# Performance work log

Measured on AMD Instinct MI355X. Metric: run time of the kernel, lower is better.

## Reference

```python
import jax, jax.numpy as jnp
import numpy as np

B, S, D, H = 1, 4096, 768, 12
HD = D // H  # 64

def setup_inputs() -> dict:
    key = jax.random.key(0)
    k1, k2, k3 = jax.random.split(key, 3)
    x = jax.random.normal(k1, (B, S, D), dtype=jnp.float32)
    W_attn = jax.random.normal(k2, (D, 3 * D), dtype=jnp.float32) * 0.02
    b_attn = jnp.zeros((3 * D,), dtype=jnp.float32)
    W_proj = jax.random.normal(k3, (D, D), dtype=jnp.float32) * 0.02
    b_proj = jnp.zeros((D,), dtype=jnp.float32)
    return {"x": x, "W_attn": W_attn, "b_attn": b_attn, "W_proj": W_proj, "b_proj": b_proj}

def reference(x, W_attn, b_attn, W_proj, b_proj):
    # qkv projection (Conv1D = x @ W + b)
    qkv = x @ W_attn + b_attn  # [B,S,3D]
    q, k, v = jnp.split(qkv, 3, axis=-1)
    def split_heads(t):
        return t.reshape(B, S, H, HD).transpose(0, 2, 1, 3)  # [B,H,S,HD]
    q, k, v = split_heads(q), split_heads(k), split_heads(v)
    # NOTE: original applies no 1/sqrt(head_dim) scaling
    scores = jnp.einsum('bhqd,bhkd->bhqk', q, k)  # [B,H,S,S]
    causal = jnp.tril(jnp.ones((S, S), dtype=bool))
    mask_value = jnp.finfo(scores.dtype).min
    scores = jnp.where(causal, scores, mask_value)
    attn = jax.nn.softmax(scores, axis=-1)
    # dropout is identity in eval mode
    out = jnp.einsum('bhqk,bhkd->bhqd', attn, v)  # [B,H,S,HD]
    out = out.transpose(0, 2, 1, 3).reshape(B, S, D)
    return out @ W_proj + b_proj
```

## Files before the change

kernel.cpp:

```cpp
#include <hip/hip_runtime.h>


typedef short bf16x8 __attribute__((ext_vector_type(8)));
typedef float f32x4 __attribute__((ext_vector_type(4)));
typedef unsigned short u16x8_t __attribute__((ext_vector_type(8)));
typedef unsigned short u16x4_t __attribute__((ext_vector_type(4)));

#define ATT_S  4096
#define ATT_D  768
#define ATT_3D 2304
#define ATT_H  12
#define LOG2E  1.44269504089f

__device__ __forceinline__ unsigned short f2b(float f) {
  union { float f; unsigned int u; } v; v.f = f;
  unsigned int r = v.u + 0x7fffu + ((v.u >> 16) & 1u);
  return (unsigned short)(r >> 16);
}
__device__ __forceinline__ float b2f(unsigned short b) {
  union { unsigned int u; float f; } v; v.u = ((unsigned int)b) << 16;
  return v.f;
}

__device__ __forceinline__ f32x4 mfma16(bf16x8 a, bf16x8 b, f32x4 c) {
  return __builtin_amdgcn_mfma_f32_16x16x32_bf16(a, b, c, 0, 0, 0);
}

__device__ __forceinline__ void glds16(const void* g, void* l) {
  __builtin_amdgcn_global_load_lds((__attribute__((address_space(1))) void*)g,
                                   (__attribute__((address_space(3))) void*)l,
                                   16, 0, 0);
}

__device__ __forceinline__ int swz8(int row, int c) {
  return row * 64 + ((c ^ (row & 7)) << 3);
}


__global__ __launch_bounds__(256) void convert_f32_bf16(
    const float* __restrict__ in, unsigned short* __restrict__ out, int n4) {
  int i = blockIdx.x * 256 + threadIdx.x;
  if (i >= n4) return;
  float4 v = ((const float4*)in)[i];
  u16x4_t o;
  o[0] = f2b(v.x); o[1] = f2b(v.y); o[2] = f2b(v.z); o[3] = f2b(v.w);
  ((u16x4_t*)out)[i] = o;
}

__global__ __launch_bounds__(256) void transpose_conv(
    const float* __restrict__ W, unsigned short* __restrict__ WT, int K, int N) {
  __shared__ float tile[32][33];
  int bx = blockIdx.x, by = blockIdx.y;
  int tx = threadIdx.x & 31, ty = threadIdx.x >> 5;
#pragma unroll
  for (int k = 0; k < 4; k++)
    tile[ty + k * 8][tx] = W[(size_t)(by * 32 + ty + k * 8) * N + bx * 32 + tx];
  __syncthreads();
#pragma unroll
  for (int k = 0; k < 4; k++)
    WT[(size_t)(bx * 32 + ty + k * 8) * K + by * 32 + tx] = f2b(tile[tx][ty + k * 8]);
}


template <int BF16_OUT>
__global__ __launch_bounds__(256) void gemm_bias(
    const unsigned short* __restrict__ A, const unsigned short* __restrict__ Bt,
    const float* __restrict__ bias, void* __restrict__ Cout,
    int M, int N, int K) {
  __shared__ unsigned short As[128 * 32];
  __shared__ unsigned short Bs[128 * 32];
  const int t = threadIdx.x;
  const int lane = t & 63;
  const int wave = t >> 6;
  const int wr = wave >> 1, wc = wave & 1;
  const int rl = lane & 15, rg = lane >> 4;

  const int nbn = N >> 7;
  const int nwg = gridDim.x;
  const int bid = blockIdx.x;
  const int cpx = nwg >> 3;
  const int swz = (bid & 7) * cpx + (bid >> 3);
  const int bm = swz / nbn, bn = swz % nbn;

  const unsigned short* Ab = A + (size_t)bm * 128 * K;
  const unsigned short* Bb = Bt + (size_t)bn * 128 * K;

  f32x4 acc[4][4];
#pragma unroll
  for (int m = 0; m < 4; m++)
#pragma unroll
    for (int n = 0; n < 4; n++) acc[m][n] = (f32x4){0.f, 0.f, 0.f, 0.f};

  for (int kt = 0; kt < K; kt += 32) {
    if (kt) __syncthreads();
#pragma unroll
    for (int it = 0; it < 2; ++it) {
      int idx = it * 256 + t;
      int row = idx >> 2;
      int slot = idx & 3;
      int sl2 = slot ^ ((row >> 1) & 3);
      unsigned short* ldsA = As + (size_t)(it * 256 + wave * 64) * 8;
      unsigned short* ldsB = Bs + (size_t)(it * 256 + wave * 64) * 8;
      glds16(Ab + (size_t)row * K + kt + sl2 * 8, ldsA);
      glds16(Bb + (size_t)row * K + kt + sl2 * 8, ldsB);
    }
    __syncthreads();

    bf16x8 a[4], b[4];
#pragma unroll
    for (int m = 0; m < 4; m++) {
      int row = wr * 64 + m * 16 + rl;
      int sl2 = rg ^ ((row >> 1) & 3);
      a[m] = *(const bf16x8*)&As[row * 32 + sl2 * 8];
    }
#pragma unroll
    for (int n = 0; n < 4; n++) {
      int row = wc * 64 + n * 16 + rl;
      int sl2 = rg ^ ((row >> 1) & 3);
      b[n] = *(const bf16x8*)&Bs[row * 32 + sl2 * 8];
    }
#pragma unroll
    for (int m = 0; m < 4; m++)
#pragma unroll
      for (int n = 0; n < 4; n++)
        acc[m][n] = mfma16(a[m], b[n], acc[m][n]);
  }

#pragma unroll
  for (int n = 0; n < 4; n++) {
    int col = bn * 128 + wc * 64 + n * 16 + rl;
    float bv = bias[col];
#pragma unroll
    for (int m = 0; m < 4; m++) {
      int row0 = bm * 128 + wr * 64 + m * 16 + rg * 4;
#pragma unroll
      for (int i = 0; i < 4; i++) {
        float v = acc[m][n][i] + bv;
        if (BF16_OUT)
          ((unsigned short*)Cout)[(size_t)(row0 + i) * N + col] = f2b(v);
        else
          ((float*)Cout)[(size_t)(row0 + i) * N + col] = v;
      }
    }
  }
}


__global__ __launch_bounds__(256) void attn_fwd(
    const unsigned short* __restrict__ qkv, unsigned short* __restrict__ aout,
    unsigned short* __restrict__ pscr, float* __restrict__ ml) {
  __shared__ unsigned short Kb[64 * 64];
  __shared__ unsigned short Vb[64 * 64];
  __shared__ unsigned short Ps[4][16 * 64];

  const int tid = threadIdx.x;
  const int lane = tid & 63;
  const int w = tid >> 6;
  const int rl = lane & 15, rg = lane >> 4;

  const int bid = blockIdx.x;
  const int h = bid % ATT_H;
  const int u = 159 - (bid / ATT_H);
  int qb, ck;
  if (u < 16)      { qb = u;                 ck = 0; }
  else if (u < 48) { qb = 16 + ((u - 16) >> 1); ck = (u - 16) & 1; }
  else if (u < 96) { qb = 32 + (u - 48) / 3;    ck = (u - 48) % 3; }
  else             { qb = 48 + ((u - 96) >> 2); ck = (u - 96) & 3; }

  const int nt = qb + 1;
  const int t0 = ck * 16;
  const int t1 = min(nt, t0 + 16);
  const int qbase = qb * 64 + w * 16;

  unsigned short* Pw = Ps[w];
  const int skey = lane >> 3;
  const int slot = lane & 7;

  bf16x8 qf[2];
#pragma unroll
  for (int ks = 0; ks < 2; ks++)
    qf[ks] = *(const bf16x8*)&qkv[(size_t)(qbase + rl) * ATT_3D + h * 64 + ks * 32 + rg * 8];

  float mS = -3.0e38f, lS = 0.f;
  f32x4 oacc[4];
#pragma unroll
  for (int hf = 0; hf < 4; hf++) oacc[hf] = (f32x4){0.f, 0.f, 0.f, 0.f};

  u16x8_t kr[2], vr[2];
  const size_t gstep = (size_t)64 * ATT_3D;
  size_t gbase = (size_t)(w * 8 + skey) * ATT_3D + 768 + h * 64 + slot * 8;

#pragma unroll
  for (int it = 0; it < 2; ++it) {
    kr[it] = *(const u16x8_t*)&qkv[gbase + (size_t)t0 * gstep + it * 32 * ATT_3D];
    vr[it] = *(const u16x8_t*)&qkv[gbase + (size_t)t0 * gstep + it * 32 * ATT_3D + 768];
  }
  {
#pragma unroll
    for (int it = 0; it < 2; ++it) {
      int key = it * 32 + w * 8 + skey;
      *(u16x8_t*)&Kb[swz8(key, slot)] = kr[it];
      *(u16x8_t*)&Pw[swz8(it * 8 + skey, slot)] = vr[it];
    }
#pragma unroll
    for (int kk = 0; kk < 2; ++kk) {
      u16x8_t g;
#pragma unroll
      for (int j = 0; j < 8; j++)
        g[j] = Pw[swz8(kk * 8 + j, lane >> 3) + (lane & 7)];
      *(u16x8_t*)&Vb[swz8(lane, kk * 4 + w)] = g;
    }
  }
  __syncthreads();

  for (int t = t0; t < t1; ++t) {
    const bool pref = (t + 1 < t1);
    if (pref) {
      size_t gb = gbase + (size_t)(t + 1) * gstep;
#pragma unroll
      for (int it = 0; it < 2; ++it) {
        kr[it] = *(const u16x8_t*)&qkv[gb + it * 32 * ATT_3D];
        vr[it] = *(const u16x8_t*)&qkv[gb + it * 32 * ATT_3D + 768];
      }
    }

    f32x4 st[4];
#pragma unroll
    for (int kf = 0; kf < 4; kf++) st[kf] = (f32x4){0.f, 0.f, 0.f, 0.f};
    __builtin_amdgcn_s_setprio(1);
#pragma unroll
    for (int ks = 0; ks < 2; ks++) {
#pragma unroll
      for (int kf = 0; kf < 4; kf++) {
        bf16x8 kfr = *(const bf16x8*)&Kb[swz8(kf * 16 + rl, ks * 4 + rg)];
        st[kf] = mfma16(kfr, qf[ks], st[kf]);
      }
    }
    __builtin_amdgcn_s_setprio(0);

    __syncthreads();
    if (pref) {
#pragma unroll
      for (int it = 0; it < 2; ++it)
        *(u16x8_t*)&Kb[swz8(it * 32 + w * 8 + skey, slot)] = kr[it];
    }

    if (t == nt - 1) {
#pragma unroll
      for (int kf = 0; kf < 4; kf++)
#pragma unroll
        for (int i = 0; i < 4; i++) {
          int key = t * 64 + kf * 16 + rg * 4 + i;
          if (key > qbase + rl) st[kf][i] = -3.0e38f;
        }
    }

    float pm = fmaxf(fmaxf(st[0][0], st[0][1]), fmaxf(st[0][2], st[0][3]));
#pragma unroll
    for (int kf = 1; kf < 4; kf++)
      pm = fmaxf(pm, fmaxf(fmaxf(st[kf][0], st[kf][1]),
                           fmaxf(st[kf][2], st[kf][3])));
    pm = fmaxf(pm, __shfl_xor(pm, 16, 64));
    pm = fmaxf(pm, __shfl_xor(pm, 32, 64));
    if (!__all(pm - mS <= 8.f)) {
      float mn = fmaxf(mS, pm);
      float fac = __expf(mS - mn);
      mS = mn;
      lS *= fac;
#pragma unroll
      for (int i = 0; i < 4; i++) {
        float fi = __shfl(fac, rg * 4 + i, 64);
#pragma unroll
        for (int hf = 0; hf < 4; hf++) oacc[hf][i] *= fi;
      }
    }
    const float mC = mS * LOG2E;
    float psum = 0.f;
#pragma unroll
    for (int kf = 0; kf < 4; kf++) {
      u16x4_t pw4;
#pragma unroll
      for (int i = 0; i < 4; i++) {
        float p = __builtin_amdgcn_exp2f(fmaf(st[kf][i], LOG2E, -mC));
        psum += p;
        pw4[i] = f2b(p);
      }
      *(u16x4_t*)&Pw[swz8(rl, kf * 2 + (rg >> 1)) + (rg & 1) * 4] = pw4;
    }
    psum += __shfl_xor(psum, 16, 64);
    psum += __shfl_xor(psum, 32, 64);
    lS += psum;

    __builtin_amdgcn_s_setprio(1);
#pragma unroll
    for (int ks2 = 0; ks2 < 2; ks2++) {
      bf16x8 pa = *(const bf16x8*)&Pw[swz8(rl, ks2 * 4 + rg)];
#pragma unroll
      for (int hf = 0; hf < 4; hf++) {
        bf16x8 vbf = *(const bf16x8*)&Vb[swz8(hf * 16 + rl, ks2 * 4 + rg)];
        oacc[hf] = mfma16(pa, vbf, oacc[hf]);
      }
    }
    __builtin_amdgcn_s_setprio(0);

    __syncthreads();
    if (pref) {
#pragma unroll
      for (int it = 0; it < 2; ++it)
        *(u16x8_t*)&Pw[swz8(it * 8 + skey, slot)] = vr[it];
#pragma unroll
      for (int kk = 0; kk < 2; ++kk) {
        u16x8_t g;
#pragma unroll
        for (int j = 0; j < 8; j++)
          g[j] = Pw[swz8(kk * 8 + j, lane >> 3) + (lane & 7)];
        *(u16x8_t*)&Vb[swz8(lane, kk * 4 + w)] = g;
      }
    }
  }

  const bool split = (qb >= 16);
  unsigned short* dst;
  int pitch;
  if (!split || ck == 0) {
    dst = aout + (size_t)(qb * 64) * ATT_D + h * 64;
    pitch = ATT_D;
  } else {
    int s;
    if (qb < 32)      s = h * 96 + (qb - 16);
    else if (qb < 48) s = h * 96 + 16 + (qb - 32) * 2 + (ck - 1);
    else              s = h * 96 + 48 + (qb - 48) * 3 + (ck - 1);
    dst = pscr + (size_t)s * 4096;
    pitch = 64;
  }
  if (split && rg == 0) {
    int unit = h * 48 + (qb - 16);
    float2* mlp = (float2*)ml;
    mlp[(unit * 4 + ck) * 64 + w * 16 + rl] = make_float2(mS, lS);
  }
#pragma unroll
  for (int i = 0; i < 4; i++) {
    float li = __shfl(lS, rg * 4 + i, 64);
    float inv = 1.f / li;
    int qrow = w * 16 + rg * 4 + i;
#pragma unroll
    for (int hf = 0; hf < 4; hf++)
      dst[(size_t)qrow * pitch + hf * 16 + rl] = f2b(oacc[hf][i] * inv);
  }
}


__global__ __launch_bounds__(256) void attn_combine(
    const unsigned short* __restrict__ pscr, const float* __restrict__ ml,
    unsigned short* __restrict__ ao) {
  const int unit = blockIdx.x;
  const int h = unit / 48, uqb = unit % 48, qb = uqb + 16;
  const int nch = (qb + 16) >> 4;
  const int tid = threadIdx.x;
  const int q = tid >> 2, part = tid & 3;

  const float2* mlp = (const float2*)ml;
  float m[4], l[4];
  float M = -3.0e38f;
  for (int c = 0; c < nch; ++c) {
    float2 p = mlp[(unit * 4 + c) * 64 + q];
    m[c] = p.x; l[c] = p.y;
    M = fmaxf(M, m[c]);
  }
  float wgt[4], den = 0.f;
  for (int c = 0; c < nch; ++c) {
    wgt[c] = l[c] * __expf(m[c] - M);
    den += wgt[c];
  }

  float acc[16];
#pragma unroll
  for (int j = 0; j < 16; j++) acc[j] = 0.f;

  unsigned short* aorow = ao + (size_t)(qb * 64 + q) * ATT_D + h * 64 + part * 16;
  for (int c = 0; c < nch; ++c) {
    const unsigned short* src;
    if (c == 0) {
      src = aorow;
    } else {
      int s;
      if (qb < 32)      s = h * 96 + (qb - 16);
      else if (qb < 48) s = h * 96 + 16 + (qb - 32) * 2 + (c - 1);
      else              s = h * 96 + 48 + (qb - 48) * 3 + (c - 1);
      src = pscr + (size_t)s * 4096 + q * 64 + part * 16;
    }
    u16x8_t v0 = *(const u16x8_t*)src;
    u16x8_t v1 = *(const u16x8_t*)(src + 8);
#pragma unroll
    for (int j = 0; j < 8; j++) acc[j] += wgt[c] * b2f(v0[j]);
#pragma unroll
    for (int j = 0; j < 8; j++) acc[8 + j] += wgt[c] * b2f(v1[j]);
  }
  float inv = 1.f / den;
  u16x8_t o0, o1;
#pragma unroll
  for (int j = 0; j < 8; j++) { o0[j] = f2b(acc[j] * inv); o1[j] = f2b(acc[8 + j] * inv); }
  *(u16x8_t*)aorow = o0;
  *(u16x8_t*)(aorow + 8) = o1;
}


extern "C" void kernel_launch(void* const* d_in, const int* in_sizes, int n_in,
                              void* d_out, int out_size, void* d_ws, size_t ws_size,
                              hipStream_t stream) {
  const float* x      = (const float*)d_in[0];
  const float* W_attn = (const float*)d_in[1];
  const float* b_attn = (const float*)d_in[2];
  const float* W_proj = (const float*)d_in[3];
  const float* b_proj = (const float*)d_in[4];
  float* out = (float*)d_out;

  char* ws = (char*)d_ws;
  unsigned short* xb  = (unsigned short*)(ws);
  unsigned short* WaT = (unsigned short*)(ws + 6291456);
  unsigned short* WpT = (unsigned short*)(ws + 9830400);
  unsigned short* qkv = (unsigned short*)(ws + 11010048);
  unsigned short* ao  = (unsigned short*)(ws + 29884416);
  unsigned short* pscr = (unsigned short*)(ws);
  float*          ml   = (float*)(ws + 9830400);

  convert_f32_bf16<<<3072, 256, 0, stream>>>(x, xb, 786432);
  transpose_conv<<<dim3(72, 24), 256, 0, stream>>>(W_attn, WaT, 768, 2304);

  gemm_bias<1><<<576, 256, 0, stream>>>(xb, WaT, b_attn, qkv, 4096, 2304, 768);
  attn_fwd<<<1920, 256, 0, stream>>>(qkv, ao, pscr, ml);
  attn_combine<<<576, 256, 0, stream>>>(pscr, ml, ao);

  transpose_conv<<<dim3(24, 24), 256, 0, stream>>>(W_proj, WpT, 768, 768);
  gemm_bias<0><<<192, 256, 0, stream>>>(ao, WpT, b_proj, out, 4096, 768, 768);
}
```

Baseline: 130.6 us.

## Make attention kernel persistent with atomic work queue and packed bf16 conversion

```diff
diff --git a/kernel.cpp b/kernel.cpp
--- a/kernel.cpp
+++ b/kernel.cpp
@@ -11,6 +11,7 @@
 #define ATT_3D 2304
 #define ATT_H  12
 #define LOG2E  1.44269504089f
+#define NUM_UNITS 1920
 
 __device__ __forceinline__ unsigned short f2b(float f) {
   union { float f; unsigned int u; } v; v.f = f;
@@ -21,6 +22,11 @@
   union { unsigned int u; float f; } v; v.u = ((unsigned int)b) << 16;
   return v.f;
 }
+__device__ __forceinline__ unsigned int cvtpk(float a, float b) {
+  unsigned int r;
+  asm("v_cvt_pk_bf16_f32 %0, %1, %2" : "=v"(r) : "v"(a), "v"(b));
+  return r;
+}
 
 __device__ __forceinline__ f32x4 mfma16(bf16x8 a, bf16x8 b, f32x4 c) {
   return __builtin_amdgcn_mfma_f32_16x16x32_bf16(a, b, c, 0, 0, 0);
@@ -30,6 +36,11 @@
   __builtin_amdgcn_global_load_lds((__attribute__((address_space(1))) void*)g,
                                    (__attribute__((address_space(3))) void*)l,
                                    16, 0, 0);
+}
+
+__device__ __forceinline__ void lbar() {
+  asm volatile("s_waitcnt lgkmcnt(0)" ::: "memory");
+  __builtin_amdgcn_s_barrier();
 }
 
 __device__ __forceinline__ int swz8(int row, int c) {
@@ -148,166 +159,67 @@
 
 __global__ __launch_bounds__(256) void attn_fwd(
     const unsigned short* __restrict__ qkv, unsigned short* __restrict__ aout,
-    unsigned short* __restrict__ pscr, float* __restrict__ ml) {
+    unsigned short* __restrict__ pscr, float* __restrict__ ml,
+    unsigned int* __restrict__ qctr) {
   __shared__ unsigned short Kb[64 * 64];
   __shared__ unsigned short Vb[64 * 64];
   __shared__ unsigned short Ps[4][16 * 64];
+  __shared__ int sticket;
 
   const int tid = threadIdx.x;
   const int lane = tid & 63;
   const int w = tid >> 6;
   const int rl = lane & 15, rg = lane >> 4;
 
-  const int bid = blockIdx.x;
-  const int h = bid % ATT_H;
-  const int u = 159 - (bid / ATT_H);
-  int qb, ck;
-  if (u < 16)      { qb = u;                 ck = 0; }
-  else if (u < 48) { qb = 16 + ((u - 16) >> 1); ck = (u - 16) & 1; }
-  else if (u < 96) { qb = 32 + (u - 48) / 3;    ck = (u - 48) % 3; }
-  else             { qb = 48 + ((u - 96) >> 2); ck = (u - 96) & 3; }
-
-  const int nt = qb + 1;
-  const int t0 = ck * 16;
-  const int t1 = min(nt, t0 + 16);
-  const int qbase = qb * 64 + w * 16;
-
   unsigned short* Pw = Ps[w];
   const int skey = lane >> 3;
   const int slot = lane & 7;
 
-  bf16x8 qf[2];
-#pragma unroll
-  for (int ks = 0; ks < 2; ks++)
-    qf[ks] = *(const bf16x8*)&qkv[(size_t)(qbase + rl) * ATT_3D + h * 64 + ks * 32 + rg * 8];
-
-  float mS = -3.0e38f, lS = 0.f;
-  f32x4 oacc[4];
-#pragma unroll
-  for (int hf = 0; hf < 4; hf++) oacc[hf] = (f32x4){0.f, 0.f, 0.f, 0.f};
-
-  u16x8_t kr[2], vr[2];
-  const size_t gstep = (size_t)64 * ATT_3D;
-  size_t gbase = (size_t)(w * 8 + skey) * ATT_3D + 768 + h * 64 + slot * 8;
-
-#pragma unroll
-  for (int it = 0; it < 2; ++it) {
-    kr[it] = *(const u16x8_t*)&qkv[gbase + (size_t)t0 * gstep + it * 32 * ATT_3D];
-    vr[it] = *(const u16x8_t*)&qkv[gbase + (size_t)t0 * gstep + it * 32 * ATT_3D + 768];
-  }
-  {
-#pragma unroll
-    for (int it = 0; it < 2; ++it) {
-      int key = it * 32 + w * 8 + skey;
-      *(u16x8_t*)&Kb[swz8(key, slot)] = kr[it];
-      *(u16x8_t*)&Pw[swz8(it * 8 + skey, slot)] = vr[it];
-    }
-#pragma unroll
-    for (int kk = 0; kk < 2; ++kk) {
-      u16x8_t g;
-#pragma unroll
-      for (int j = 0; j < 8; j++)
-        g[j] = Pw[swz8(kk * 8 + j, lane >> 3) + (lane & 7)];
-      *(u16x8_t*)&Vb[swz8(lane, kk * 4 + w)] = g;
-    }
-  }
-  __syncthreads();
-
-  for (int t = t0; t < t1; ++t) {
-    const bool pref = (t + 1 < t1);
-    if (pref) {
-      size_t gb = gbase + (size_t)(t + 1) * gstep;
+  for (;;) {
+    if (tid == 0) sticket = (int)atomicAdd(qctr, 1u);
+    __syncthreads();
+    const int tk = sticket;
+    if (tk >= NUM_UNITS) return;
+
+    const int h = tk % ATT_H;
+    const int u = 159 - (tk / ATT_H);
+    int qb, ck;
+    if (u < 16)      { qb = u;                    ck = 0; }
+    else if (u < 48) { qb = 16 + ((u - 16) >> 1); ck = (u - 16) & 1; }
+    else if (u < 96) { qb = 32 + (u - 48) / 3;    ck = (u - 48) % 3; }
+    else             { qb = 48 + ((u - 96) >> 2); ck = (u - 96) & 3; }
+
+    const int nt = qb + 1;
+    const int t0 = ck * 16;
+    const int t1 = min(nt, t0 + 16);
+    const int qbase = qb * 64 + w * 16;
+
+    bf16x8 qf[2];
+#pragma unroll
+    for (int ks = 0; ks < 2; ks++)
+      qf[ks] = *(const bf16x8*)&qkv[(size_t)(qbase + rl) * ATT_3D + h * 64 + ks * 32 + rg * 8];
+
+    float mS = -3.0e38f, lS = 0.f;
+    f32x4 oacc[4];
+#pragma unroll
+    for (int hf = 0; hf < 4; hf++) oacc[hf] = (f32x4){0.f, 0.f, 0.f, 0.f};
+
+    u16x8_t kr[2], vr[2];
+    const size_t gstep = (size_t)64 * ATT_3D;
+    const size_t gbase = (size_t)(w * 8 + skey) * ATT_3D + 768 + h * 64 + slot * 8;
+
+    {
+      const size_t gb = gbase + (size_t)t0 * gstep;
+      kr[0] = *(const u16x8_t*)&qkv[gb];
+      kr[1] = *(const u16x8_t*)&qkv[gb + 32 * ATT_3D];
+      vr[0] = *(const u16x8_t*)&qkv[gb + 768];
+      vr[1] = *(const u16x8_t*)&qkv[gb + 32 * ATT_3D + 768];
 #pragma unroll
       for (int it = 0; it < 2; ++it) {
-        kr[it] = *(const u16x8_t*)&qkv[gb + it * 32 * ATT_3D];
-        vr[it] = *(const u16x8_t*)&qkv[gb + it * 32 * ATT_3D + 768];
-      }
-    }
-
-    f32x4 st[4];
-#pragma unroll
-    for (int kf = 0; kf < 4; kf++) st[kf] = (f32x4){0.f, 0.f, 0.f, 0.f};
-    __builtin_amdgcn_s_setprio(1);
-#pragma unroll
-    for (int ks = 0; ks < 2; ks++) {
-#pragma unroll
-      for (int kf = 0; kf < 4; kf++) {
-        bf16x8 kfr = *(const bf16x8*)&Kb[swz8(kf * 16 + rl, ks * 4 + rg)];
-        st[kf] = mfma16(kfr, qf[ks], st[kf]);
-      }
-    }
-    __builtin_amdgcn_s_setprio(0);
-
-    __syncthreads();
-    if (pref) {
-#pragma unroll
-      for (int it = 0; it < 2; ++it)
-        *(u16x8_t*)&Kb[swz8(it * 32 + w * 8 + skey, slot)] = kr[it];
-    }
-
-    if (t == nt - 1) {
-#pragma unroll
-      for (int kf = 0; kf < 4; kf++)
-#pragma unroll
-        for (int i = 0; i < 4; i++) {
-          int key = t * 64 + kf * 16 + rg * 4 + i;
-          if (key > qbase + rl) st[kf][i] = -3.0e38f;
-        }
-    }
-
-    float pm = fmaxf(fmaxf(st[0][0], st[0][1]), fmaxf(st[0][2], st[0][3]));
-#pragma unroll
-    for (int kf = 1; kf < 4; kf++)
-      pm = fmaxf(pm, fmaxf(fmaxf(st[kf][0], st[kf][1]),
-                           fmaxf(st[kf][2], st[kf][3])));
-    pm = fmaxf(pm, __shfl_xor(pm, 16, 64));
-    pm = fmaxf(pm, __shfl_xor(pm, 32, 64));
-    if (!__all(pm - mS <= 8.f)) {
-      float mn = fmaxf(mS, pm);
-      float fac = __expf(mS - mn);
-      mS = mn;
-      lS *= fac;
-#pragma unroll
-      for (int i = 0; i < 4; i++) {
-        float fi = __shfl(fac, rg * 4 + i, 64);
-#pragma unroll
-        for (int hf = 0; hf < 4; hf++) oacc[hf][i] *= fi;
-      }
-    }
-    const float mC = mS * LOG2E;
-    float psum = 0.f;
-#pragma unroll
-    for (int kf = 0; kf < 4; kf++) {
-      u16x4_t pw4;
-#pragma unroll
-      for (int i = 0; i < 4; i++) {
-        float p = __builtin_amdgcn_exp2f(fmaf(st[kf][i], LOG2E, -mC));
-        psum += p;
-        pw4[i] = f2b(p);
-      }
-      *(u16x4_t*)&Pw[swz8(rl, kf * 2 + (rg >> 1)) + (rg & 1) * 4] = pw4;
-    }
-    psum += __shfl_xor(psum, 16, 64);
-    psum += __shfl_xor(psum, 32, 64);
-    lS += psum;
-
-    __builtin_amdgcn_s_setprio(1);
-#pragma unroll
-    for (int ks2 = 0; ks2 < 2; ks2++) {
-      bf16x8 pa = *(const bf16x8*)&Pw[swz8(rl, ks2 * 4 + rg)];
-#pragma unroll
-      for (int hf = 0; hf < 4; hf++) {
-        bf16x8 vbf = *(const bf16x8*)&Vb[swz8(hf * 16 + rl, ks2 * 4 + rg)];
-        oacc[hf] = mfma16(pa, vbf, oacc[hf]);
-      }
-    }
-    __builtin_amdgcn_s_setprio(0);
-
-    __syncthreads();
-    if (pref) {
-#pragma unroll
-      for (int it = 0; it < 2; ++it)
+        int key = it * 32 + w * 8 + skey;
+        *(u16x8_t*)&Kb[swz8(key, slot)] = kr[it];
         *(u16x8_t*)&Pw[swz8(it * 8 + skey, slot)] = vr[it];
+      }
 #pragma unroll
       for (int kk = 0; kk < 2; ++kk) {
         u16x8_t g;
@@ -317,35 +229,144 @@
         *(u16x8_t*)&Vb[swz8(lane, kk * 4 + w)] = g;
       }
     }
-  }
-
-  const bool split = (qb >= 16);
-  unsigned short* dst;
-  int pitch;
-  if (!split || ck == 0) {
-    dst = aout + (size_t)(qb * 64) * ATT_D + h * 64;
-    pitch = ATT_D;
-  } else {
-    int s;
-    if (qb < 32)      s = h * 96 + (qb - 16);
-    else if (qb < 48) s = h * 96 + 16 + (qb - 32) * 2 + (ck - 1);
-    else              s = h * 96 + 48 + (qb - 48) * 3 + (ck - 1);
-    dst = pscr + (size_t)s * 4096;
-    pitch = 64;
-  }
-  if (split && rg == 0) {
-    int unit = h * 48 + (qb - 16);
-    float2* mlp = (float2*)ml;
-    mlp[(unit * 4 + ck) * 64 + w * 16 + rl] = make_float2(mS, lS);
-  }
-#pragma unroll
-  for (int i = 0; i < 4; i++) {
-    float li = __shfl(lS, rg * 4 + i, 64);
-    float inv = 1.f / li;
-    int qrow = w * 16 + rg * 4 + i;
-#pragma unroll
-    for (int hf = 0; hf < 4; hf++)
-      dst[(size_t)qrow * pitch + hf * 16 + rl] = f2b(oacc[hf][i] * inv);
+    lbar();
+
+    for (int t = t0; t < t1; ++t) {
+      const bool pref = (t + 1 < t1);
+      if (pref) {
+        const size_t gb = gbase + (size_t)(t + 1) * gstep;
+        kr[0] = *(const u16x8_t*)&qkv[gb];
+        kr[1] = *(const u16x8_t*)&qkv[gb + 32 * ATT_3D];
+        vr[0] = *(const u16x8_t*)&qkv[gb + 768];
+        vr[1] = *(const u16x8_t*)&qkv[gb + 32 * ATT_3D + 768];
+      }
+
+      f32x4 st[4];
+#pragma unroll
+      for (int kf = 0; kf < 4; kf++) st[kf] = (f32x4){0.f, 0.f, 0.f, 0.f};
+      __builtin_amdgcn_s_setprio(1);
+#pragma unroll
+      for (int ks = 0; ks < 2; ks++) {
+#pragma unroll
+        for (int kf = 0; kf < 4; kf++) {
+          bf16x8 kfr = *(const bf16x8*)&Kb[swz8(kf * 16 + rl, ks * 4 + rg)];
+          st[kf] = mfma16(kfr, qf[ks], st[kf]);
+        }
+      }
+      __builtin_amdgcn_s_setprio(0);
+
+      lbar();
+      if (pref) {
+#pragma unroll
+        for (int it = 0; it < 2; ++it)
+          *(u16x8_t*)&Kb[swz8(it * 32 + w * 8 + skey, slot)] = kr[it];
+      }
+
+      if (t == nt - 1) {
+#pragma unroll
+        for (int kf = 0; kf < 4; kf++)
+#pragma unroll
+          for (int i = 0; i < 4; i++) {
+            int key = t * 64 + kf * 16 + rg * 4 + i;
+            if (key > qbase + rl) st[kf][i] = -3.0e38f;
+          }
+      }
+
+      float pm = fmaxf(fmaxf(st[0][0], st[0][1]), fmaxf(st[0][2], st[0][3]));
+#pragma unroll
+      for (int kf = 1; kf < 4; kf++)
+        pm = fmaxf(pm, fmaxf(fmaxf(st[kf][0], st[kf][1]),
+                             fmaxf(st[kf][2], st[kf][3])));
+      pm = fmaxf(pm, __shfl_xor(pm, 16, 64));
+      pm = fmaxf(pm, __shfl_xor(pm, 32, 64));
+      if (!__all(pm - mS <= 8.f)) {
+        float mn = fmaxf(mS, pm);
+        float fac = __expf(mS - mn);
+        mS = mn;
+        lS *= fac;
+#pragma unroll
+        for (int i = 0; i < 4; i++) {
+          float fi = __shfl(fac, rg * 4 + i, 64);
+#pragma unroll
+          for (int hf = 0; hf < 4; hf++) oacc[hf][i] *= fi;
+        }
+      }
+      const float mC = mS * LOG2E;
+      float psum = 0.f;
+#pragma unroll
+      for (int kf = 0; kf < 4; kf++) {
+        float p0 = __builtin_amdgcn_exp2f(fmaf(st[kf][0], LOG2E, -mC));
+        float p1 = __builtin_amdgcn_exp2f(fmaf(st[kf][1], LOG2E, -mC));
+        float p2 = __builtin_amdgcn_exp2f(fmaf(st[kf][2], LOG2E, -mC));
+        float p3 = __builtin_amdgcn_exp2f(fmaf(st[kf][3], LOG2E, -mC));
+        psum += (p0 + p1) + (p2 + p3);
+        uint2 d;
+        d.x = cvtpk(p0, p1);
+        d.y = cvtpk(p2, p3);
+        *(u16x4_t*)&Pw[swz8(rl, kf * 2 + (rg >> 1)) + (rg & 1) * 4] =
+            __builtin_bit_cast(u16x4_t, d);
+      }
+      psum += __shfl_xor(psum, 16, 64);
+      psum += __shfl_xor(psum, 32, 64);
+      lS += psum;
+
+      __builtin_amdgcn_s_setprio(1);
+#pragma unroll
+      for (int ks2 = 0; ks2 < 2; ks2++) {
+        bf16x8 pa = *(const bf16x8*)&Pw[swz8(rl, ks2 * 4 + rg)];
+#pragma unroll
+        for (int hf = 0; hf < 4; hf++) {
+          bf16x8 vbf = *(const bf16x8*)&Vb[swz8(hf * 16 + rl, ks2 * 4 + rg)];
+          oacc[hf] = mfma16(pa, vbf, oacc[hf]);
+        }
+      }
+      __builtin_amdgcn_s_setprio(0);
+
+      lbar();
+      if (pref) {
+#pragma unroll
+        for (int it = 0; it < 2; ++it)
+          *(u16x8_t*)&Pw[swz8(it * 8 + skey, slot)] = vr[it];
+#pragma unroll
+        for (int kk = 0; kk < 2; ++kk) {
+          u16x8_t g;
+#pragma unroll
+          for (int j = 0; j < 8; j++)
+            g[j] = Pw[swz8(kk * 8 + j, lane >> 3) + (lane & 7)];
+          *(u16x8_t*)&Vb[swz8(lane, kk * 4 + w)] = g;
+        }
+      }
+    }
+
+    const bool split = (qb >= 16);
+    unsigned short* dst;
+    int pitch;
+    if (!split || ck == 0) {
+      dst = aout + (size_t)(qb * 64) * ATT_D + h * 64;
+      pitch = ATT_D;
+    } else {
+      int s;
+      if (qb < 32)      s = h * 96 + (qb - 16);
+      else if (qb < 48) s = h * 96 + 16 + (qb - 32) * 2 + (ck - 1);
+      else              s = h * 96 + 48 + (qb - 48) * 3 + (ck - 1);
+      dst = pscr + (size_t)s * 4096;
+      pitch = 64;
+    }
+    if (split && rg == 0) {
+      int unit = h * 48 + (qb - 16);
+      float2* mlp = (float2*)ml;
+      mlp[(unit * 4 + ck) * 64 + w * 16 + rl] = make_float2(mS, lS);
+    }
+#pragma unroll
+    for (int i = 0; i < 4; i++) {
+      float li = __shfl(lS, rg * 4 + i, 64);
+      float inv = 1.f / li;
+      int qrow = w * 16 + rg * 4 + i;
+#pragma unroll
+      for (int hf = 0; hf < 4; hf++)
+        dst[(size_t)qrow * pitch + hf * 16 + rl] = f2b(oacc[hf][i] * inv);
+    }
+    __syncthreads();
   }
 }
 
@@ -422,13 +443,15 @@
   unsigned short* qkv = (unsigned short*)(ws + 11010048);
   unsigned short* ao  = (unsigned short*)(ws + 29884416);
   unsigned short* pscr = (unsigned short*)(ws);
+  unsigned int*   qctr = (unsigned int*)(ws + 9437184);
   float*          ml   = (float*)(ws + 9830400);
 
   convert_f32_bf16<<<3072, 256, 0, stream>>>(x, xb, 786432);
   transpose_conv<<<dim3(72, 24), 256, 0, stream>>>(W_attn, WaT, 768, 2304);
 
   gemm_bias<1><<<576, 256, 0, stream>>>(xb, WaT, b_attn, qkv, 4096, 2304, 768);
-  attn_fwd<<<1920, 256, 0, stream>>>(qkv, ao, pscr, ml);
+  hipMemsetAsync(qctr, 0, 4, stream);
+  attn_fwd<<<1536, 256, 0, stream>>>(qkv, ao, pscr, ml, qctr);
   attn_combine<<<576, 256, 0, stream>>>(pscr, ml, ao);
 
   transpose_conv<<<dim3(24, 24), 256, 0, stream>>>(W_proj, WpT, 768, 768);
```

Measured after the change: 149.1 us. 1.14x slower.
